# Optimization experiments

Hardware: AMD Instinct MI355X
Metric: run time of the kernel (lower is better)

## Reference

```python
import jax, jax.numpy as jnp
import numpy as np

BETA_MEM = 0.9
BETA_INH = 0.6
THRESHOLD = 1.0
SURR_ALPHA = 2.0  # snntorch default ATan surrogate alpha


@jax.custom_vjp
def spike_fn(x):
    # Heaviside spike with ATan surrogate gradient (snntorch default).
    return (x > 0).astype(x.dtype)


def _spike_fwd(x):
    return spike_fn(x), x


def _spike_bwd(x, g):
    # d/dx ATan surrogate: alpha/2 / (1 + (pi/2 * alpha * x)^2); alpha=2 -> 1/(1+(pi*x)^2)
    pi_half_alpha = jnp.float32(np.pi / 2.0 * SURR_ALPHA)
    grad = (SURR_ALPHA / 2.0) / (1.0 + (pi_half_alpha * x) ** 2)
    return (g * grad.astype(x.dtype),)


spike_fn.defvjp(_spike_fwd, _spike_bwd)


def setup_inputs() -> dict:
    key = jax.random.key(0)
    k1, = jax.random.split(key, 1)
    T, B = 4096, 4096
    # Bernoulli(0.05) spike trains on the two input channels (FM1, FM3)
    spike_seq = (jax.random.uniform(k1, (T, B, 2)) < 0.05).astype(jnp.float32)
    # fc_exc weight pinned to [[0, 1]] in the original module
    w_exc = jnp.array([[0.0, 1.0]], dtype=jnp.float32)
    # inhibitory weight parameter initialized to 0.0
    w_inh = jnp.float32(0.0)
    return {"spike_seq": spike_seq, "w_exc": w_exc, "w_inh": w_inh}


def reference(spike_seq, w_exc, w_inh):
    T, B, _ = spike_seq.shape
    mem0 = jnp.zeros((B, 1), dtype=spike_seq.dtype)
    inh0 = jnp.zeros((B, 1), dtype=spike_seq.dtype)

    def step(carry, x_t):
        mem, inh_state = carry
        cur_exc = x_t @ w_exc.T                       # [B,1]
        fm1_t = x_t[:, 0:1]                           # [B,1]
        inh_state = BETA_INH * inh_state + fm1_t
        cur_inh = w_inh * inh_state
        cur = cur_exc + cur_inh
        # snntorch Leaky (reset-by-subtraction): reset uses spike of PREVIOUS mem
        reset = spike_fn(mem - THRESHOLD)
        mem_new = BETA_MEM * mem + cur - reset * THRESHOLD
        spk = spike_fn(mem_new - THRESHOLD)
        return (mem_new, inh_state), (spk, cur_exc, cur_inh, mem_new)

    _, (spk_rec, exc_rec, inh_rec, mem_rec) = jax.lax.scan(step, (mem0, inh0), spike_seq)
    return spk_rec, exc_rec, inh_rec, mem_rec
```

## Files before the change

kernel.cpp:

```cpp
#include <hip/hip_runtime.h>
#include <stdint.h>

#define T_STEPS 4096
#define B_SIZE  4096
#define NWORDS  (T_STEPS / 32)
#define B2      (B_SIZE / 2)
#define B4      (B_SIZE / 4)

typedef float    f32x4 __attribute__((ext_vector_type(4)));
typedef uint32_t u32x4 __attribute__((ext_vector_type(4)));
typedef uint32_t u32x2 __attribute__((ext_vector_type(2)));


__device__ __forceinline__ float bitf(uint32_t w, int k) {
    return (float)((w >> k) & 1u);
}

__global__ __launch_bounds__(256) void k_pack(const f32x4* __restrict__ x,
                                              u32x2* __restrict__ p0,
                                              u32x2* __restrict__ p1) {
    uint32_t gid = blockIdx.x * 256u + threadIdx.x;
    uint32_t i  = gid >> 11;
    uint32_t bp = gid & (B2 - 1);
    const f32x4* xp = x + (size_t)i * 32u * B2 + bp;
    uint32_t e0 = 0u, e1 = 0u, o0 = 0u, o1 = 0u;
#pragma unroll
    for (int k = 0; k < 32; ++k) {
        f32x4 v = __builtin_nontemporal_load(xp + (size_t)k * B2);
        e0 |= ((uint32_t)(v.x != 0.0f)) << k;
        e1 |= ((uint32_t)(v.y != 0.0f)) << k;
        o0 |= ((uint32_t)(v.z != 0.0f)) << k;
        o1 |= ((uint32_t)(v.w != 0.0f)) << k;
    }
    u32x2 s0; s0.x = e0; s0.y = o0;
    u32x2 s1; s1.x = e1; s1.y = o1;
    p0[(size_t)i * B2 + bp] = s0;
    p1[(size_t)i * B2 + bp] = s1;
}

__global__ __launch_bounds__(64) void k_scan(const uint32_t* __restrict__ p0,
                                             const uint32_t* __restrict__ p1,
                                             const float* __restrict__ w_exc,
                                             const float* __restrict__ w_inh_p,
                                             float* __restrict__ mem_ck,
                                             float* __restrict__ inh_ck) {
    int b = blockIdx.x * 64 + threadIdx.x;
    const float w00 = w_exc[0], w01 = w_exc[1], winh = w_inh_p[0];
    float mem = 0.0f, inh = 0.0f;

    if (w00 == 0.0f && winh == 0.0f) {
        uint32_t c0 = p1[b];
        uint32_t c1 = p1[(size_t)1 * B_SIZE + b];
        uint32_t c2 = p1[(size_t)2 * B_SIZE + b];
        uint32_t c3 = p1[(size_t)3 * B_SIZE + b];
        for (int i = 0; i < NWORDS; i += 4) {
            uint32_t n0 = 0u, n1 = 0u, n2 = 0u, n3 = 0u;
            if (i + 4 < NWORDS) {
                n0 = p1[(size_t)(i + 4) * B_SIZE + b];
                n1 = p1[(size_t)(i + 5) * B_SIZE + b];
                n2 = p1[(size_t)(i + 6) * B_SIZE + b];
                n3 = p1[(size_t)(i + 7) * B_SIZE + b];
            }
            uint32_t ws[4] = {c0, c1, c2, c3};
#pragma unroll
            for (int j = 0; j < 4; ++j) {
                mem_ck[(size_t)(i + j) * B_SIZE + b] = mem;
                uint32_t w1 = ws[j];
#pragma unroll
                for (int k = 0; k < 32; ++k) {
                    float x1f = bitf(w1, k);
                    float r   = (mem > 1.0f) ? 1.0f : 0.0f;
                    float m1  = __fmul_rn(0.9f, mem);
                    float m2  = __fmaf_rn(x1f, w01, m1);
                    mem       = __fsub_rn(m2, r);
                }
            }
            c0 = n0; c1 = n1; c2 = n2; c3 = n3;
        }
    } else {
        uint32_t a0 = p0[b];
        uint32_t a1 = p0[(size_t)1 * B_SIZE + b];
        uint32_t a2 = p0[(size_t)2 * B_SIZE + b];
        uint32_t a3 = p0[(size_t)3 * B_SIZE + b];
        uint32_t c0 = p1[b];
        uint32_t c1 = p1[(size_t)1 * B_SIZE + b];
        uint32_t c2 = p1[(size_t)2 * B_SIZE + b];
        uint32_t c3 = p1[(size_t)3 * B_SIZE + b];
        for (int i = 0; i < NWORDS; i += 4) {
            uint32_t m0 = 0u, m1_ = 0u, m2_ = 0u, m3 = 0u;
            uint32_t n0 = 0u, n1 = 0u, n2 = 0u, n3 = 0u;
            if (i + 4 < NWORDS) {
                m0 = p0[(size_t)(i + 4) * B_SIZE + b];
                m1_ = p0[(size_t)(i + 5) * B_SIZE + b];
                m2_ = p0[(size_t)(i + 6) * B_SIZE + b];
                m3 = p0[(size_t)(i + 7) * B_SIZE + b];
                n0 = p1[(size_t)(i + 4) * B_SIZE + b];
                n1 = p1[(size_t)(i + 5) * B_SIZE + b];
                n2 = p1[(size_t)(i + 6) * B_SIZE + b];
                n3 = p1[(size_t)(i + 7) * B_SIZE + b];
            }
            uint32_t wa[4] = {a0, a1, a2, a3};
            uint32_t wc[4] = {c0, c1, c2, c3};
#pragma unroll
            for (int j = 0; j < 4; ++j) {
                mem_ck[(size_t)(i + j) * B_SIZE + b] = mem;
                inh_ck[(size_t)(i + j) * B_SIZE + b] = inh;
                uint32_t w0 = wa[j], w1 = wc[j];
#pragma unroll
                for (int k = 0; k < 32; ++k) {
                    float x0f = bitf(w0, k);
                    float x1f = bitf(w1, k);
                    float exc = __fadd_rn(__fmul_rn(x0f, w00), __fmul_rn(x1f, w01));
                    inh       = __fadd_rn(__fmul_rn(0.6f, inh), x0f);
                    float ci  = __fmul_rn(winh, inh);
                    float cur = __fadd_rn(exc, ci);
                    float r   = (mem > 1.0f) ? 1.0f : 0.0f;
                    float mm1 = __fmul_rn(0.9f, mem);
                    float mm2 = __fadd_rn(mm1, cur);
                    mem       = __fsub_rn(mm2, r);
                }
            }
            a0 = m0; a1 = m1_; a2 = m2_; a3 = m3;
            c0 = n0; c1 = n1; c2 = n2; c3 = n3;
        }
    }
}

__global__ __launch_bounds__(256) void k_replay(const uint32_t* __restrict__ p0,
                                                const uint32_t* __restrict__ p1,
                                                const float* __restrict__ w_exc,
                                                const float* __restrict__ w_inh_p,
                                                const float* __restrict__ mem_ck,
                                                const float* __restrict__ inh_ck,
                                                float* __restrict__ out) {
    uint32_t gid = blockIdx.x * 256u + threadIdx.x;
    uint32_t i = gid >> 10;
    uint32_t q = gid & (B4 - 1);
    f32x4* __restrict__ spk4 = (f32x4*)out;
    f32x4* __restrict__ exc4 = (f32x4*)(out + (size_t)T_STEPS * B_SIZE);
    f32x4* __restrict__ inh4 = (f32x4*)(out + 2 * (size_t)T_STEPS * B_SIZE);
    f32x4* __restrict__ mem4 = (f32x4*)(out + 3 * (size_t)T_STEPS * B_SIZE);
    const float w00 = w_exc[0], w01 = w_exc[1], winh = w_inh_p[0];

    f32x4 mem = ((const f32x4*)mem_ck)[(size_t)i * B4 + q];
    u32x4 w1q = ((const u32x4*)p1)[(size_t)i * B4 + q];
    size_t base = (size_t)i * 32u * B4 + q;

    if (w00 == 0.0f && winh == 0.0f) {
        f32x4 z4; z4.x = 0.0f; z4.y = 0.0f; z4.z = 0.0f; z4.w = 0.0f;
#pragma unroll
        for (int k = 0; k < 32; ++k) {
            f32x4 exc, spk;
#define STEPF(C, W)                                                          \
            {                                                                \
                float x1f = bitf(W, k);                                      \
                float r   = (mem.C > 1.0f) ? 1.0f : 0.0f;                    \
                exc.C = __fmul_rn(x1f, w01);                                 \
                mem.C = __fsub_rn(__fmaf_rn(x1f, w01, __fmul_rn(0.9f, mem.C)), r); \
                spk.C = (mem.C > 1.0f) ? 1.0f : 0.0f;                        \
            }
            STEPF(x, w1q.x) STEPF(y, w1q.y) STEPF(z, w1q.z) STEPF(w, w1q.w)
#undef STEPF
            size_t idx = base + (size_t)k * B4;
            __builtin_nontemporal_store(spk, spk4 + idx);
            __builtin_nontemporal_store(exc, exc4 + idx);
            __builtin_nontemporal_store(z4,  inh4 + idx);
            __builtin_nontemporal_store(mem, mem4 + idx);
        }
    } else {
        f32x4 inh = ((const f32x4*)inh_ck)[(size_t)i * B4 + q];
        u32x4 w0q = ((const u32x4*)p0)[(size_t)i * B4 + q];
#pragma unroll
        for (int k = 0; k < 32; ++k) {
            f32x4 excv, civ, spkv;
#define STEP(C)                                                              \
            {                                                                \
                float x0f = bitf(w0q.C, k);                                  \
                float x1f = bitf(w1q.C, k);                                  \
                float exc = __fadd_rn(__fmul_rn(x0f, w00), __fmul_rn(x1f, w01)); \
                inh.C     = __fadd_rn(__fmul_rn(0.6f, inh.C), x0f);          \
                float ci  = __fmul_rn(winh, inh.C);                          \
                float cur = __fadd_rn(exc, ci);                              \
                float r   = (mem.C > 1.0f) ? 1.0f : 0.0f;                    \
                mem.C     = __fsub_rn(__fadd_rn(__fmul_rn(0.9f, mem.C), cur), r); \
                excv.C = exc; civ.C = ci;                                    \
                spkv.C = (mem.C > 1.0f) ? 1.0f : 0.0f;                       \
            }
            STEP(x) STEP(y) STEP(z) STEP(w)
#undef STEP
            size_t idx = base + (size_t)k * B4;
            __builtin_nontemporal_store(spkv, spk4 + idx);
            __builtin_nontemporal_store(excv, exc4 + idx);
            __builtin_nontemporal_store(civ,  inh4 + idx);
            __builtin_nontemporal_store(mem,  mem4 + idx);
        }
    }
}

__global__ __launch_bounds__(256) void k_naive(const float2* __restrict__ x,
                                               const float* __restrict__ w_exc,
                                               const float* __restrict__ w_inh_p,
                                               float* __restrict__ out) {
    int b = blockIdx.x * 256 + threadIdx.x;
    const float w00 = w_exc[0], w01 = w_exc[1], winh = w_inh_p[0];
    float* __restrict__ spk_o = out;
    float* __restrict__ exc_o = out + (size_t)T_STEPS * B_SIZE;
    float* __restrict__ inh_o = out + 2 * (size_t)T_STEPS * B_SIZE;
    float* __restrict__ mem_o = out + 3 * (size_t)T_STEPS * B_SIZE;
    float mem = 0.0f, inh = 0.0f;
    for (int t = 0; t < T_STEPS; ++t) {
        float2 v = x[(size_t)t * B_SIZE + b];
        float exc = __fadd_rn(__fmul_rn(v.x, w00), __fmul_rn(v.y, w01));
        inh       = __fadd_rn(__fmul_rn(0.6f, inh), v.x);
        float ci  = __fmul_rn(winh, inh);
        float cur = __fadd_rn(exc, ci);
        float r   = (mem > 1.0f) ? 1.0f : 0.0f;
        float m1  = __fmul_rn(0.9f, mem);
        mem       = __fsub_rn(__fadd_rn(m1, cur), r);
        float spk = (mem > 1.0f) ? 1.0f : 0.0f;
        size_t idx = (size_t)t * B_SIZE + b;
        spk_o[idx] = spk; exc_o[idx] = exc; inh_o[idx] = ci; mem_o[idx] = mem;
    }
}

extern "C" void kernel_launch(void* const* d_in, const int* in_sizes, int n_in,
                              void* d_out, int out_size, void* d_ws, size_t ws_size,
                              hipStream_t stream) {
    const f32x4*  x4     = (const f32x4*)d_in[0];
    const float*  w_exc  = (const float*)d_in[1];
    const float*  w_inh  = (const float*)d_in[2];
    float* out = (float*)d_out;

    const size_t nw = (size_t)NWORDS * B_SIZE;
    const size_t need = nw * (sizeof(uint32_t) * 2 + sizeof(float) * 2);

    if (ws_size >= need) {
        uint32_t* p0     = (uint32_t*)d_ws;
        uint32_t* p1     = p0 + nw;
        float*    mem_ck = (float*)(p1 + nw);
        float*    inh_ck = mem_ck + nw;

        k_pack<<<(NWORDS * B2) / 256, 256, 0, stream>>>(x4, (u32x2*)p0, (u32x2*)p1);
        k_scan<<<B_SIZE / 64, 64, 0, stream>>>(p0, p1, w_exc, w_inh, mem_ck, inh_ck);
        k_replay<<<(NWORDS * B4) / 256, 256, 0, stream>>>(p0, p1, w_exc, w_inh,
                                                          mem_ck, inh_ck, out);
    } else {
        k_naive<<<B_SIZE / 256, 256, 0, stream>>>((const float2*)d_in[0], w_exc, w_inh, out);
    }
}
```

Before: 432.4 us.

## Fuse pack and scan into one launch, scanning directly from raw float input

Merges the bit-packing kernel and the sequential scan kernel into one launch. The first 16 blocks run the per-batch scan straight from the float input, double-buffering 32 timesteps in registers, while the remaining blocks do the bit packing in parallel. The sequential scan no longer waits for packing to finish, and the packing traffic overlaps with it. In exchange the scan threads read the full float input (8 bytes per step instead of packed bits) and hold large register buffers. Only 16 blocks of 256 threads carry the serial chain, so they occupy few CUs.

Result: slower. 587.2 us (+35.8%).

```diff
diff --git a/kernel.cpp b/kernel.cpp
--- a/kernel.cpp
+++ b/kernel.cpp
@@ -3,126 +3,95 @@
 
 #define T_STEPS 4096
 #define B_SIZE  4096
-#define NWORDS  (T_STEPS / 32)
-#define B2      (B_SIZE / 2)
-#define B4      (B_SIZE / 4)
+#define NWORDS  128
+#define B2      2048
+#define B4      1024
 
 typedef float    f32x4 __attribute__((ext_vector_type(4)));
+typedef float    f32x2 __attribute__((ext_vector_type(2)));
 typedef uint32_t u32x4 __attribute__((ext_vector_type(4)));
 typedef uint32_t u32x2 __attribute__((ext_vector_type(2)));
 
-
 __device__ __forceinline__ float bitf(uint32_t w, int k) {
     return (float)((w >> k) & 1u);
 }
 
-__global__ __launch_bounds__(256) void k_pack(const f32x4* __restrict__ x,
-                                              u32x2* __restrict__ p0,
-                                              u32x2* __restrict__ p1) {
-    uint32_t gid = blockIdx.x * 256u + threadIdx.x;
-    uint32_t i  = gid >> 11;
-    uint32_t bp = gid & (B2 - 1);
-    const f32x4* xp = x + (size_t)i * 32u * B2 + bp;
-    uint32_t e0 = 0u, e1 = 0u, o0 = 0u, o1 = 0u;
-#pragma unroll
-    for (int k = 0; k < 32; ++k) {
-        f32x4 v = __builtin_nontemporal_load(xp + (size_t)k * B2);
-        e0 |= ((uint32_t)(v.x != 0.0f)) << k;
-        e1 |= ((uint32_t)(v.y != 0.0f)) << k;
-        o0 |= ((uint32_t)(v.z != 0.0f)) << k;
-        o1 |= ((uint32_t)(v.w != 0.0f)) << k;
-    }
-    u32x2 s0; s0.x = e0; s0.y = o0;
-    u32x2 s1; s1.x = e1; s1.y = o1;
-    p0[(size_t)i * B2 + bp] = s0;
-    p1[(size_t)i * B2 + bp] = s1;
-}
-
-__global__ __launch_bounds__(64) void k_scan(const uint32_t* __restrict__ p0,
-                                             const uint32_t* __restrict__ p1,
-                                             const float* __restrict__ w_exc,
-                                             const float* __restrict__ w_inh_p,
-                                             float* __restrict__ mem_ck,
-                                             float* __restrict__ inh_ck) {
-    int b = blockIdx.x * 64 + threadIdx.x;
+__global__ __launch_bounds__(256) void k_packscan(
+        const f32x4* __restrict__ x,
+        const float* __restrict__ w_exc,
+        const float* __restrict__ w_inh_p,
+        u32x2* __restrict__ p0, u32x2* __restrict__ p1,
+        float* __restrict__ mem_ck, float* __restrict__ inh_ck)
+{
+    const uint32_t bk = blockIdx.x, t = threadIdx.x;
     const float w00 = w_exc[0], w01 = w_exc[1], winh = w_inh_p[0];
-    float mem = 0.0f, inh = 0.0f;
-
-    if (w00 == 0.0f && winh == 0.0f) {
-        uint32_t c0 = p1[b];
-        uint32_t c1 = p1[(size_t)1 * B_SIZE + b];
-        uint32_t c2 = p1[(size_t)2 * B_SIZE + b];
-        uint32_t c3 = p1[(size_t)3 * B_SIZE + b];
-        for (int i = 0; i < NWORDS; i += 4) {
-            uint32_t n0 = 0u, n1 = 0u, n2 = 0u, n3 = 0u;
-            if (i + 4 < NWORDS) {
-                n0 = p1[(size_t)(i + 4) * B_SIZE + b];
-                n1 = p1[(size_t)(i + 5) * B_SIZE + b];
-                n2 = p1[(size_t)(i + 6) * B_SIZE + b];
-                n3 = p1[(size_t)(i + 7) * B_SIZE + b];
+    const bool fast = (w00 == 0.0f && winh == 0.0f);
+
+    if (bk < 16u) {
+        const int b = (int)(bk * 256u + t);
+        const f32x2* xb = (const f32x2*)x;
+        float mem = 0.0f, inh = 0.0f;
+        f32x2 bufA[32], bufB[32];
+
+#pragma unroll
+        for (int k = 0; k < 32; ++k)
+            bufA[k] = xb[(size_t)k * B_SIZE + b];
+
+#define SCAN_STEP(V)                                                         \
+        {                                                                    \
+            float x0f = (V).x, x1f = (V).y;                                  \
+            if (fast) {                                                      \
+                float r  = (mem > 1.0f) ? 1.0f : 0.0f;                       \
+                float m1 = __fmul_rn(0.9f, mem);                             \
+                mem      = __fsub_rn(__fmaf_rn(x1f, w01, m1), r);            \
+            } else {                                                         \
+                float exc = __fadd_rn(__fmul_rn(x0f, w00), __fmul_rn(x1f, w01)); \
+                inh       = __fadd_rn(__fmul_rn(0.6f, inh), x0f);            \
+                float ci  = __fmul_rn(winh, inh);                            \
+                float cur = __fadd_rn(exc, ci);                              \
+                float r   = (mem > 1.0f) ? 1.0f : 0.0f;                      \
+                mem       = __fsub_rn(__fadd_rn(__fmul_rn(0.9f, mem), cur), r); \
+            }                                                                \
+        }
+
+        for (int i = 0; i < NWORDS; i += 2) {
+#pragma unroll
+            for (int k = 0; k < 32; ++k)
+                bufB[k] = xb[((size_t)(i + 1) * 32 + k) * B_SIZE + b];
+            mem_ck[(size_t)i * B_SIZE + b] = mem;
+            if (!fast) inh_ck[(size_t)i * B_SIZE + b] = inh;
+#pragma unroll
+            for (int k = 0; k < 32; ++k) SCAN_STEP(bufA[k]);
+
+            if (i + 2 < NWORDS) {
+#pragma unroll
+                for (int k = 0; k < 32; ++k)
+                    bufA[k] = xb[((size_t)(i + 2) * 32 + k) * B_SIZE + b];
             }
-            uint32_t ws[4] = {c0, c1, c2, c3};
-#pragma unroll
-            for (int j = 0; j < 4; ++j) {
-                mem_ck[(size_t)(i + j) * B_SIZE + b] = mem;
-                uint32_t w1 = ws[j];
-#pragma unroll
-                for (int k = 0; k < 32; ++k) {
-                    float x1f = bitf(w1, k);
-                    float r   = (mem > 1.0f) ? 1.0f : 0.0f;
-                    float m1  = __fmul_rn(0.9f, mem);
-                    float m2  = __fmaf_rn(x1f, w01, m1);
-                    mem       = __fsub_rn(m2, r);
-                }
-            }
-            c0 = n0; c1 = n1; c2 = n2; c3 = n3;
-        }
+            mem_ck[(size_t)(i + 1) * B_SIZE + b] = mem;
+            if (!fast) inh_ck[(size_t)(i + 1) * B_SIZE + b] = inh;
+#pragma unroll
+            for (int k = 0; k < 32; ++k) SCAN_STEP(bufB[k]);
+        }
+#undef SCAN_STEP
     } else {
-        uint32_t a0 = p0[b];
-        uint32_t a1 = p0[(size_t)1 * B_SIZE + b];
-        uint32_t a2 = p0[(size_t)2 * B_SIZE + b];
-        uint32_t a3 = p0[(size_t)3 * B_SIZE + b];
-        uint32_t c0 = p1[b];
-        uint32_t c1 = p1[(size_t)1 * B_SIZE + b];
-        uint32_t c2 = p1[(size_t)2 * B_SIZE + b];
-        uint32_t c3 = p1[(size_t)3 * B_SIZE + b];
-        for (int i = 0; i < NWORDS; i += 4) {
-            uint32_t m0 = 0u, m1_ = 0u, m2_ = 0u, m3 = 0u;
-            uint32_t n0 = 0u, n1 = 0u, n2 = 0u, n3 = 0u;
-            if (i + 4 < NWORDS) {
-                m0 = p0[(size_t)(i + 4) * B_SIZE + b];
-                m1_ = p0[(size_t)(i + 5) * B_SIZE + b];
-                m2_ = p0[(size_t)(i + 6) * B_SIZE + b];
-                m3 = p0[(size_t)(i + 7) * B_SIZE + b];
-                n0 = p1[(size_t)(i + 4) * B_SIZE + b];
-                n1 = p1[(size_t)(i + 5) * B_SIZE + b];
-                n2 = p1[(size_t)(i + 6) * B_SIZE + b];
-                n3 = p1[(size_t)(i + 7) * B_SIZE + b];
-            }
-            uint32_t wa[4] = {a0, a1, a2, a3};
-            uint32_t wc[4] = {c0, c1, c2, c3};
-#pragma unroll
-            for (int j = 0; j < 4; ++j) {
-                mem_ck[(size_t)(i + j) * B_SIZE + b] = mem;
-                inh_ck[(size_t)(i + j) * B_SIZE + b] = inh;
-                uint32_t w0 = wa[j], w1 = wc[j];
-#pragma unroll
-                for (int k = 0; k < 32; ++k) {
-                    float x0f = bitf(w0, k);
-                    float x1f = bitf(w1, k);
-                    float exc = __fadd_rn(__fmul_rn(x0f, w00), __fmul_rn(x1f, w01));
-                    inh       = __fadd_rn(__fmul_rn(0.6f, inh), x0f);
-                    float ci  = __fmul_rn(winh, inh);
-                    float cur = __fadd_rn(exc, ci);
-                    float r   = (mem > 1.0f) ? 1.0f : 0.0f;
-                    float mm1 = __fmul_rn(0.9f, mem);
-                    float mm2 = __fadd_rn(mm1, cur);
-                    mem       = __fsub_rn(mm2, r);
-                }
-            }
-            a0 = m0; a1 = m1_; a2 = m2_; a3 = m3;
-            c0 = n0; c1 = n1; c2 = n2; c3 = n3;
-        }
+        uint32_t gid = (bk - 16u) * 256u + t;
+        uint32_t i  = gid >> 11;
+        uint32_t bp = gid & (B2 - 1u);
+        const f32x4* xp = x + (size_t)i * 32u * B2 + bp;
+        uint32_t e0 = 0u, e1 = 0u, o0 = 0u, o1 = 0u;
+#pragma unroll
+        for (int k = 0; k < 32; ++k) {
+            f32x4 v = __builtin_nontemporal_load(xp + (size_t)k * B2);
+            e0 |= ((uint32_t)(v.x != 0.0f)) << k;
+            e1 |= ((uint32_t)(v.y != 0.0f)) << k;
+            o0 |= ((uint32_t)(v.z != 0.0f)) << k;
+            o1 |= ((uint32_t)(v.w != 0.0f)) << k;
+        }
+        u32x2 s0; s0.x = e0; s0.y = o0;
+        u32x2 s1; s1.x = e1; s1.y = o1;
+        p0[(size_t)i * B2 + bp] = s0;
+        p1[(size_t)i * B2 + bp] = s1;
     }
 }
 
@@ -141,7 +110,6 @@
     f32x4* __restrict__ inh4 = (f32x4*)(out + 2 * (size_t)T_STEPS * B_SIZE);
     f32x4* __restrict__ mem4 = (f32x4*)(out + 3 * (size_t)T_STEPS * B_SIZE);
     const float w00 = w_exc[0], w01 = w_exc[1], winh = w_inh_p[0];
-
     f32x4 mem = ((const f32x4*)mem_ck)[(size_t)i * B4 + q];
     u32x4 w1q = ((const u32x4*)p1)[(size_t)i * B4 + q];
     size_t base = (size_t)i * 32u * B4 + q;
@@ -215,8 +183,7 @@
         float ci  = __fmul_rn(winh, inh);
         float cur = __fadd_rn(exc, ci);
         float r   = (mem > 1.0f) ? 1.0f : 0.0f;
-        float m1  = __fmul_rn(0.9f, mem);
-        mem       = __fsub_rn(__fadd_rn(m1, cur), r);
+        mem       = __fsub_rn(__fadd_rn(__fmul_rn(0.9f, mem), cur), r);
         float spk = (mem > 1.0f) ? 1.0f : 0.0f;
         size_t idx = (size_t)t * B_SIZE + b;
         spk_o[idx] = spk; exc_o[idx] = exc; inh_o[idx] = ci; mem_o[idx] = mem;
@@ -232,16 +199,15 @@
     float* out = (float*)d_out;
 
     const size_t nw = (size_t)NWORDS * B_SIZE;
-    const size_t need = nw * (sizeof(uint32_t) * 2 + sizeof(float) * 2);
+    uint32_t* p0     = (uint32_t*)d_ws;
+    uint32_t* p1     = p0 + nw;
+    float*    mem_ck = (float*)(p1 + nw);
+    float*    inh_ck = mem_ck + nw;
+    const size_t need = nw * 16;
 
     if (ws_size >= need) {
-        uint32_t* p0     = (uint32_t*)d_ws;
-        uint32_t* p1     = p0 + nw;
-        float*    mem_ck = (float*)(p1 + nw);
-        float*    inh_ck = mem_ck + nw;
-
-        k_pack<<<(NWORDS * B2) / 256, 256, 0, stream>>>(x4, (u32x2*)p0, (u32x2*)p1);
-        k_scan<<<B_SIZE / 64, 64, 0, stream>>>(p0, p1, w_exc, w_inh, mem_ck, inh_ck);
+        k_packscan<<<16 + (NWORDS * B2) / 256, 256, 0, stream>>>(
+            x4, w_exc, w_inh, (u32x2*)p0, (u32x2*)p1, mem_ck, inh_ck);
         k_replay<<<(NWORDS * B4) / 256, 256, 0, stream>>>(p0, p1, w_exc, w_inh,
                                                           mem_ck, inh_ck, out);
     } else {
```
